# Performance work log

Hardware: AMD Instinct MI355X
Metric: run time of the kernel (lower is better)

## Reference

```python
import jax, jax.numpy as jnp
import numpy as np

N, F_IN, HID, H1, E = 50000, 512, 128, 4, 800000
NEG_SLOPE = 0.2

def setup_inputs() -> dict:
    key = jax.random.key(0)
    ks = jax.random.split(key, 10)
    s = lambda fan: 1.0 / np.sqrt(fan)
    x = jax.random.normal(ks[0], (N, F_IN), jnp.float32)
    edge_index = jax.random.randint(ks[1], (2, E), 0, N, jnp.int32)
    W1 = jax.random.normal(ks[2], (F_IN, H1 * HID), jnp.float32) * s(F_IN)
    a_src1 = jax.random.normal(ks[3], (H1, HID), jnp.float32) * s(HID)
    a_dst1 = jax.random.normal(ks[4], (H1, HID), jnp.float32) * s(HID)
    b1 = jnp.zeros((H1 * HID,), jnp.float32)
    W2 = jax.random.normal(ks[5], (H1 * HID, HID), jnp.float32) * s(H1 * HID)
    a_src2 = jax.random.normal(ks[6], (1, HID), jnp.float32) * s(HID)
    a_dst2 = jax.random.normal(ks[7], (1, HID), jnp.float32) * s(HID)
    b2 = jnp.zeros((HID,), jnp.float32)
    return {"x": x, "edge_index": edge_index, "W1": W1, "a_src1": a_src1,
            "a_dst1": a_dst1, "b1": b1, "W2": W2, "a_src2": a_src2,
            "a_dst2": a_dst2, "b2": b2}

def _gat(x, src, dst, W, a_src, a_dst, b, n):
    H, C = a_src.shape
    h = (x @ W).reshape(-1, H, C)                      # [N, H, C]
    # per-edge attention logits: alpha_src[src] + alpha_dst[dst]
    e = jax.nn.leaky_relu((h * a_src).sum(-1)[src] + (h * a_dst).sum(-1)[dst],
                          NEG_SLOPE)                   # [E', H]
    # segment softmax over destination node
    m = jax.ops.segment_max(e, dst, num_segments=n)
    p = jnp.exp(e - m[dst])
    denom = jax.ops.segment_sum(p, dst, num_segments=n)
    alpha = p / (denom[dst] + 1e-16)
    # weighted scatter-add aggregation
    out = jax.ops.segment_sum(h[src] * alpha[:, :, None], dst, num_segments=n)
    return out.reshape(-1, H * C) + b

def reference(x, edge_index, W1, a_src1, a_dst1, b1, W2, a_src2, a_dst2, b2):
    loops = jnp.arange(N, dtype=edge_index.dtype)      # add_self_loops=True
    src = jnp.concatenate([edge_index[0], loops])
    dst = jnp.concatenate([edge_index[1], loops])
    h = jax.nn.elu(_gat(x, src, dst, W1, a_src1, a_dst1, b1, N))
    return _gat(h, src, dst, W2, a_src2, a_dst2, b2, N)
```

## Files before the change

kernel.cpp:

```cpp
#include <hip/hip_runtime.h>
#include <hip/hip_bf16.h>
#include <math.h>

#define NEG_SLOPE 0.2f

constexpr int N_NODES = 50000;
constexpr int F_IN    = 512;
constexpr int HID     = 128;
constexpr int H1      = 4;
constexpr int E_EDGES = 800000;
constexpr int E_TOT   = E_EDGES + N_NODES;
constexpr int DEG_CAP = 64;

typedef __attribute__((ext_vector_type(8))) short short8;
typedef __attribute__((ext_vector_type(4))) float floatx4;
typedef __attribute__((ext_vector_type(2))) float f32x2;
typedef __attribute__((ext_vector_type(4))) unsigned short ushort4v;
typedef __attribute__((ext_vector_type(8))) unsigned short ushort8v;

__device__ __forceinline__ unsigned short f2bf(float f) {
  union { float f; unsigned int u; } v; v.f = f;
  unsigned int u = v.u + 0x7FFFu + ((v.u >> 16) & 1u);
  return (unsigned short)(u >> 16);
}
__device__ __forceinline__ float bf_lo(unsigned int u) {
  union { unsigned int u; float f; } v; v.u = u << 16; return v.f;
}
__device__ __forceinline__ float bf_hi(unsigned int u) {
  union { unsigned int u; float f; } v; v.u = u & 0xFFFF0000u; return v.f;
}

template <int CPT>
__device__ __forceinline__ void store_vec(unsigned short* p, const float* v) {
#pragma unroll
  for (int c = 0; c < CPT; c += 4) {
    ushort4v o;
#pragma unroll
    for (int j = 0; j < 4; ++j) o[j] = f2bf(v[c + j]);
    *(ushort4v*)(p + c) = o;
  }
}
template <int CPT>
__device__ __forceinline__ void store_vec(float* p, const float* v) {
#pragma unroll
  for (int c = 0; c < CPT; c += 4) *(float4*)(p + c) = *(const float4*)(v + c);
}

__device__ __forceinline__ void async_load16(const void* g, void* lds) {
  __builtin_amdgcn_global_load_lds(
      (const __attribute__((address_space(1))) unsigned int*)g,
      (__attribute__((address_space(3))) unsigned int*)lds, 16, 0, 0);
}

__global__ void prep_kernel(const float* __restrict__ W1, const float* __restrict__ W2,
                            unsigned short* __restrict__ W1t, unsigned short* __restrict__ W2t,
                            int* __restrict__ cnt) {
  int i = blockIdx.x * 256 + threadIdx.x;
  if (i < N_NODES) cnt[i] = 0;
  int j = i - N_NODES;
  if (j >= 0 && j < 512 * 512) {
    int n = j >> 9, k = j & 511;
    W1t[j] = f2bf(W1[k * 512 + n]);
  }
  int l = i - N_NODES - 512 * 512;
  if (l >= 0 && l < 128 * 512) {
    int n = l >> 9, k = l & 511;
    W2t[l] = f2bf(W2[k * 128 + n]);
  }
}

template <bool CVT_A, bool FILL>
__global__ __launch_bounds__(256) void gemm_bf16_kernel(
    const void* __restrict__ Araw, const unsigned short* __restrict__ Bt,
    unsigned short* __restrict__ C, const float* __restrict__ a_srcp,
    const float* __restrict__ a_dstp,
    float* __restrict__ alpha_src, float* __restrict__ alpha_dst,
    int M, int N, int K, int Hn, int nRowTiles,
    const int* __restrict__ ei, int* __restrict__ cnt, int* __restrict__ adj,
    int gemmBlocks) {
  __shared__ unsigned short As[128 * 32];
  __shared__ unsigned short Bs[128 * 32];
  __shared__ unsigned short Cs[128 * 132];
  __shared__ float red_s[128][2];
  __shared__ float red_d[128][2];

  if (FILL && blockIdx.x >= gemmBlocks) {
    int i = (blockIdx.x - gemmBlocks) * 256 + threadIdx.x;
    if (i < E_TOT) {
      int s, d;
      if (i < E_EDGES) { s = ei[i]; d = ei[E_EDGES + i]; }
      else             { s = i - E_EDGES; d = s; }
      int pos = atomicAdd(&cnt[d], 1);
      if (pos < DEG_CAP) adj[d * DEG_CAP + pos] = s;
    }
    return;
  }

  int grp = blockIdx.x / (8 * Hn);
  int w8 = blockIdx.x % (8 * Hn);
  int head = w8 >> 3;
  int rowTile = grp * 8 + (w8 & 7);
  if (rowTile >= nRowTiles) return;
  int row0 = rowTile * 128;
  int col0 = head * 128;

  int tid = threadIdx.x;
  int lane = tid & 63, wave = tid >> 6;
  int wm = wave & 1, wn = wave >> 1;
  int l15 = lane & 15, quad = lane >> 4;

  floatx4 acc[4][4];
#pragma unroll
  for (int i = 0; i < 4; ++i)
#pragma unroll
    for (int j = 0; j < 4; ++j) acc[i][j] = (floatx4){0.f, 0.f, 0.f, 0.f};

  int seg_b = wave * 2;
  int r_in = (lane >> 2);
  int c8sw = (((lane & 3) ^ ((lane >> 3) & 3)) * 8);
  int sqrd = (quad ^ ((l15 >> 1) & 3)) * 8;

  for (int k0 = 0; k0 < K; k0 += 32) {
#pragma unroll
    for (int p = 0; p < 2; ++p) {
      int seg = seg_b + p;
      int r = seg * 16 + r_in;
      int gc = col0 + r;
      async_load16(Bt + (size_t)gc * K + k0 + c8sw, &Bs[seg * 512]);
    }
    if constexpr (CVT_A) {
      const float* Af = (const float*)Araw;
#pragma unroll
      for (int p = 0; p < 4; ++p) {
        int lin = tid + p * 256;
        int r = lin >> 3;
        int q = lin & 7;
        int gr = row0 + r; if (gr >= M) gr = M - 1;
        float4 f = *(const float4*)(Af + (size_t)gr * K + k0 + q * 4);
        ushort4v o;
        o[0] = f2bf(f.x); o[1] = f2bf(f.y); o[2] = f2bf(f.z); o[3] = f2bf(f.w);
        int sl = ((q >> 1) ^ ((lin >> 4) & 3));
        *(ushort4v*)&As[r * 32 + sl * 8 + (q & 1) * 4] = o;
      }
    } else {
      const unsigned short* Ab = (const unsigned short*)Araw;
#pragma unroll
      for (int p = 0; p < 2; ++p) {
        int seg = seg_b + p;
        int r = seg * 16 + r_in;
        int gr = row0 + r; if (gr >= M) gr = M - 1;
        async_load16(Ab + (size_t)gr * K + k0 + c8sw, &As[seg * 512]);
      }
    }
    __syncthreads();

    short8 a[4], b[4];
#pragma unroll
    for (int mi = 0; mi < 4; ++mi)
      a[mi] = *(const short8*)&As[(wm * 64 + mi * 16 + l15) * 32 + sqrd];
#pragma unroll
    for (int ni = 0; ni < 4; ++ni)
      b[ni] = *(const short8*)&Bs[(wn * 64 + ni * 16 + l15) * 32 + sqrd];
#pragma unroll
    for (int mi = 0; mi < 4; ++mi)
#pragma unroll
      for (int ni = 0; ni < 4; ++ni)
        acc[mi][ni] = __builtin_amdgcn_mfma_f32_16x16x32_bf16(a[mi], b[ni], acc[mi][ni], 0, 0, 0);
    __syncthreads();
  }

  float a_s[4], a_d[4];
#pragma unroll
  for (int ni = 0; ni < 4; ++ni) {
    int cih = wn * 64 + ni * 16 + l15;
    a_s[ni] = a_srcp[head * HID + cih];
    a_d[ni] = a_dstp[head * HID + cih];
  }

#pragma unroll
  for (int mi = 0; mi < 4; ++mi) {
#pragma unroll
    for (int r = 0; r < 4; ++r) {
      int rloc = wm * 64 + mi * 16 + quad * 4 + r;
      float ps = 0.f, pd = 0.f;
#pragma unroll
      for (int ni = 0; ni < 4; ++ni) {
        float v = acc[mi][ni][r];
        ps += v * a_s[ni];
        pd += v * a_d[ni];
        Cs[rloc * 132 + wn * 64 + ni * 16 + l15] = f2bf(v);
      }
#pragma unroll
      for (int off = 1; off < 16; off <<= 1) {
        ps += __shfl_xor(ps, off);
        pd += __shfl_xor(pd, off);
      }
      if (l15 == 0) { red_s[rloc][wn] = ps; red_d[rloc][wn] = pd; }
    }
  }
  __syncthreads();

  {
    int row = tid >> 1;
    int cc  = (tid & 1) * 64;
    int grow = row0 + row;
    if (grow < M) {
      const unsigned short* src = &Cs[row * 132 + cc];
      unsigned short* dst = &C[(size_t)grow * N + col0 + cc];
#pragma unroll
      for (int c = 0; c < 64; c += 8)
        *(ushort8v*)(dst + c) = *(const ushort8v*)(src + c);
    }
  }
  if (tid < 128) {
    int grow = row0 + tid;
    if (grow < M) {
      alpha_src[(size_t)grow * Hn + head] = red_s[tid][0] + red_s[tid][1];
      alpha_dst[(size_t)grow * Hn + head] = red_d[tid][0] + red_d[tid][1];
    }
  }
}

template <int H, typename OT>
__global__ __launch_bounds__(64) void aggregate_kernel(
    const unsigned short* __restrict__ h, const float* __restrict__ asrc,
    const float* __restrict__ adst, const int* __restrict__ cnt,
    const int* __restrict__ adj, const float* __restrict__ bias,
    OT* __restrict__ out, int apply_elu) {
  constexpr int CPT = 8;
  constexpr int CH = H * HID;
  constexpr int NCH = CH / CPT;
  constexpr int SLOTS = 64 / NCH;
  __shared__ float p_sh[64 * H];
  __shared__ int ro_sh[64];

  const int node = blockIdx.x;
  const int lane = threadIdx.x;
  int deg = cnt[node];
  if (deg > DEG_CAP) deg = DEG_CAP;

  int s_i = 0;
  if (lane < deg) s_i = adj[node * DEG_CAP + lane];
  ro_sh[lane] = s_i * (CH * 2);
  float ar[H];
  if constexpr (H == 4) {
    float4 f = (lane < deg) ? *(const float4*)(asrc + (size_t)s_i * 4)
                            : make_float4(0.f, 0.f, 0.f, 0.f);
    ar[0] = f.x; ar[1] = f.y; ar[2] = f.z; ar[3] = f.w;
  } else {
    ar[0] = (lane < deg) ? asrc[s_i] : 0.f;
  }
  asm volatile("s_waitcnt lgkmcnt(0)" ::: "memory");

  const int chlane = lane % NCH;
  const int slot = lane / NCH;
  const int ch = chlane * CPT;
  const int head = ch >> 7;
  const char* hb = (const char*)h + ch * 2;

  auto loadu = [&](uint4& U, int e) {
    if (e < deg) U = *(const uint4*)(hb + (unsigned)ro_sh[e]);
    else         U = make_uint4(0u, 0u, 0u, 0u);
  };

  uint4 u0, u1, u2, u3, u4, u5, u6, u7;
  loadu(u0, slot);             loadu(u1, slot + SLOTS);
  loadu(u2, slot + 2 * SLOTS); loadu(u3, slot + 3 * SLOTS);
  loadu(u4, slot + 4 * SLOTS); loadu(u5, slot + 5 * SLOTS);
  loadu(u6, slot + 6 * SLOTS); loadu(u7, slot + 7 * SLOTS);

#pragma unroll
  for (int hh = 0; hh < H; ++hh) {
    float v = ar[hh] + adst[node * H + hh];
    v = (v > 0.f) ? v : NEG_SLOPE * v;
    float lg = (lane < deg) ? v : -1e30f;
#pragma unroll
    for (int o = 32; o; o >>= 1) lg = fmaxf(lg, __shfl_xor(lg, o));
    float p = (lane < deg) ? __expf(v - lg) : 0.f;
    float s = p;
#pragma unroll
    for (int o = 32; o; o >>= 1) s += __shfl_xor(s, o);
    p_sh[lane * H + hh] = p * (1.f / (s + 1e-16f));
  }
  asm volatile("s_waitcnt lgkmcnt(0)" ::: "memory");

  f32x2 ac0 = {0.f, 0.f}, ac1 = {0.f, 0.f}, ac2v = {0.f, 0.f}, ac3 = {0.f, 0.f};
  auto consume = [&](const uint4& U, int e) {
    float w = p_sh[(e & 63) * H + head];
    f32x2 wp = {w, w};
    f32x2 t;
    t.x = bf_lo(U.x); t.y = bf_hi(U.x); ac0  += t * wp;
    t.x = bf_lo(U.y); t.y = bf_hi(U.y); ac1  += t * wp;
    t.x = bf_lo(U.z); t.y = bf_hi(U.z); ac2v += t * wp;
    t.x = bf_lo(U.w); t.y = bf_hi(U.w); ac3  += t * wp;
  };

  int base = 0;
  for (;;) {
    int nb = base + 8 * SLOTS;
    if (nb < deg) {
      consume(u0, base + slot);             loadu(u0, nb + slot);
      consume(u1, base + slot + SLOTS);     loadu(u1, nb + slot + SLOTS);
      consume(u2, base + slot + 2 * SLOTS); loadu(u2, nb + slot + 2 * SLOTS);
      consume(u3, base + slot + 3 * SLOTS); loadu(u3, nb + slot + 3 * SLOTS);
      consume(u4, base + slot + 4 * SLOTS); loadu(u4, nb + slot + 4 * SLOTS);
      consume(u5, base + slot + 5 * SLOTS); loadu(u5, nb + slot + 5 * SLOTS);
      consume(u6, base + slot + 6 * SLOTS); loadu(u6, nb + slot + 6 * SLOTS);
      consume(u7, base + slot + 7 * SLOTS); loadu(u7, nb + slot + 7 * SLOTS);
      base = nb;
    } else {
      consume(u0, base + slot);             consume(u1, base + slot + SLOTS);
      consume(u2, base + slot + 2 * SLOTS); consume(u3, base + slot + 3 * SLOTS);
      consume(u4, base + slot + 4 * SLOTS); consume(u5, base + slot + 5 * SLOTS);
      consume(u6, base + slot + 6 * SLOTS); consume(u7, base + slot + 7 * SLOTS);
      break;
    }
  }

#pragma unroll
  for (int o = NCH; o < 64; o <<= 1) {
    ac0.x  += __shfl_xor(ac0.x, o);  ac0.y  += __shfl_xor(ac0.y, o);
    ac1.x  += __shfl_xor(ac1.x, o);  ac1.y  += __shfl_xor(ac1.y, o);
    ac2v.x += __shfl_xor(ac2v.x, o); ac2v.y += __shfl_xor(ac2v.y, o);
    ac3.x  += __shfl_xor(ac3.x, o);  ac3.y  += __shfl_xor(ac3.y, o);
  }

  if (slot == 0) {
    float r[CPT] = {ac0.x, ac0.y, ac1.x, ac1.y, ac2v.x, ac2v.y, ac3.x, ac3.y};
#pragma unroll
    for (int c = 0; c < CPT; ++c) {
      float t = r[c] + bias[ch + c];
      if (apply_elu) t = (t > 0.f) ? t : (__expf(t) - 1.f);
      r[c] = t;
    }
    store_vec<CPT>(&out[(size_t)node * CH + ch], r);
  }
}

extern "C" void kernel_launch(void* const* d_in, const int* in_sizes, int n_in,
                              void* d_out, int out_size, void* d_ws, size_t ws_size,
                              hipStream_t stream) {
  const float* x      = (const float*)d_in[0];
  const int*   ei     = (const int*)d_in[1];
  const float* W1     = (const float*)d_in[2];
  const float* a_src1 = (const float*)d_in[3];
  const float* a_dst1 = (const float*)d_in[4];
  const float* b1     = (const float*)d_in[5];
  const float* W2     = (const float*)d_in[6];
  const float* a_src2 = (const float*)d_in[7];
  const float* a_dst2 = (const float*)d_in[8];
  const float* b2     = (const float*)d_in[9];
  float* out = (float*)d_out;

  float* ws   = (float*)d_ws;
  float* as1  = ws;
  float* ad1  = as1 + N_NODES * H1;
  float* as2  = ad1 + N_NODES * H1;
  float* ad2  = as2 + N_NODES;
  unsigned short* bufA = (unsigned short*)(ad2 + N_NODES);
  unsigned short* bufB = bufA + (size_t)N_NODES * 512;
  unsigned short* hmidb = bufA;
  unsigned short* h1b   = bufB;
  unsigned short* h2b   = bufB;
  unsigned short* W1t   = bufB + (size_t)N_NODES * 512;
  unsigned short* W2t   = W1t + 512 * 512;
  int* cnt = (int*)(W2t + 128 * 512);
  int* adj = cnt + N_NODES;

  constexpr int NRT = (N_NODES + 127) / 128;
  constexpr int NRT8 = ((NRT + 7) / 8) * 8;
  constexpr int PREP_ITEMS = N_NODES + 512 * 512 + 128 * 512;
  constexpr int FILL_BLOCKS = (E_TOT + 255) / 256;
  constexpr int GEMM1_BLOCKS = NRT8 * H1;

  prep_kernel<<<(PREP_ITEMS + 255) / 256, 256, 0, stream>>>(W1, W2, W1t, W2t, cnt);

  gemm_bf16_kernel<true, true>
      <<<GEMM1_BLOCKS + FILL_BLOCKS, 256, 0, stream>>>(
      x, W1t, h1b, a_src1, a_dst1, as1, ad1, N_NODES, 512, 512, H1, NRT,
      ei, cnt, adj, GEMM1_BLOCKS);
  aggregate_kernel<4, unsigned short><<<N_NODES, 64, 0, stream>>>(
      h1b, as1, ad1, cnt, adj, b1, hmidb, 1);

  gemm_bf16_kernel<false, false><<<NRT8, 256, 0, stream>>>(
      hmidb, W2t, h2b, a_src2, a_dst2, as2, ad2, N_NODES, 128, 512, 1, NRT,
      nullptr, nullptr, nullptr, 0);
  aggregate_kernel<1, float><<<N_NODES, 64, 0, stream>>>(
      h2b, as2, ad2, cnt, adj, b2, out, 0);
}
```

Before: 464.0 us.

## Pre-convert x to bf16 in prep kernel and alias GEMM LDS buffers

```diff
diff --git a/kernel.cpp b/kernel.cpp
--- a/kernel.cpp
+++ b/kernel.cpp
@@ -52,35 +52,51 @@
       (__attribute__((address_space(3))) unsigned int*)lds, 16, 0, 0);
 }
 
-__global__ void prep_kernel(const float* __restrict__ W1, const float* __restrict__ W2,
+constexpr int XC8 = N_NODES * F_IN / 8;
+__global__ void prep_kernel(const float* __restrict__ x, unsigned short* __restrict__ xb,
+                            const float* __restrict__ W1, const float* __restrict__ W2,
                             unsigned short* __restrict__ W1t, unsigned short* __restrict__ W2t,
                             int* __restrict__ cnt) {
   int i = blockIdx.x * 256 + threadIdx.x;
-  if (i < N_NODES) cnt[i] = 0;
-  int j = i - N_NODES;
-  if (j >= 0 && j < 512 * 512) {
+  if (i < XC8) {
+    int i8 = i * 8;
+    float4 f0 = *(const float4*)(x + i8);
+    float4 f1 = *(const float4*)(x + i8 + 4);
+    ushort8v o;
+    o[0] = f2bf(f0.x); o[1] = f2bf(f0.y); o[2] = f2bf(f0.z); o[3] = f2bf(f0.w);
+    o[4] = f2bf(f1.x); o[5] = f2bf(f1.y); o[6] = f2bf(f1.z); o[7] = f2bf(f1.w);
+    *(ushort8v*)(xb + i8) = o;
+    return;
+  }
+  int j = i - XC8;
+  if (j < 512 * 512) {
     int n = j >> 9, k = j & 511;
     W1t[j] = f2bf(W1[k * 512 + n]);
-  }
-  int l = i - N_NODES - 512 * 512;
-  if (l >= 0 && l < 128 * 512) {
+    return;
+  }
+  int l = j - 512 * 512;
+  if (l < 128 * 512) {
     int n = l >> 9, k = l & 511;
     W2t[l] = f2bf(W2[k * 128 + n]);
-  }
-}
-
-template <bool CVT_A, bool FILL>
+    return;
+  }
+  int c = l - 128 * 512;
+  if (c < N_NODES) cnt[c] = 0;
+}
+
+template <bool FILL>
 __global__ __launch_bounds__(256) void gemm_bf16_kernel(
-    const void* __restrict__ Araw, const unsigned short* __restrict__ Bt,
+    const unsigned short* __restrict__ A, const unsigned short* __restrict__ Bt,
     unsigned short* __restrict__ C, const float* __restrict__ a_srcp,
     const float* __restrict__ a_dstp,
     float* __restrict__ alpha_src, float* __restrict__ alpha_dst,
     int M, int N, int K, int Hn, int nRowTiles,
     const int* __restrict__ ei, int* __restrict__ cnt, int* __restrict__ adj,
     int gemmBlocks) {
-  __shared__ unsigned short As[128 * 32];
-  __shared__ unsigned short Bs[128 * 32];
-  __shared__ unsigned short Cs[128 * 132];
+  __shared__ __align__(16) unsigned char smem[128 * 132 * 2];
+  unsigned short* As = (unsigned short*)smem;
+  unsigned short* Bs = (unsigned short*)(smem + 8192);
+  unsigned short* Cs = (unsigned short*)smem;
   __shared__ float red_s[128][2];
   __shared__ float red_d[128][2];
 
@@ -128,29 +144,12 @@
       int gc = col0 + r;
       async_load16(Bt + (size_t)gc * K + k0 + c8sw, &Bs[seg * 512]);
     }
-    if constexpr (CVT_A) {
-      const float* Af = (const float*)Araw;
-#pragma unroll
-      for (int p = 0; p < 4; ++p) {
-        int lin = tid + p * 256;
-        int r = lin >> 3;
-        int q = lin & 7;
-        int gr = row0 + r; if (gr >= M) gr = M - 1;
-        float4 f = *(const float4*)(Af + (size_t)gr * K + k0 + q * 4);
-        ushort4v o;
-        o[0] = f2bf(f.x); o[1] = f2bf(f.y); o[2] = f2bf(f.z); o[3] = f2bf(f.w);
-        int sl = ((q >> 1) ^ ((lin >> 4) & 3));
-        *(ushort4v*)&As[r * 32 + sl * 8 + (q & 1) * 4] = o;
-      }
-    } else {
-      const unsigned short* Ab = (const unsigned short*)Araw;
-#pragma unroll
-      for (int p = 0; p < 2; ++p) {
-        int seg = seg_b + p;
-        int r = seg * 16 + r_in;
-        int gr = row0 + r; if (gr >= M) gr = M - 1;
-        async_load16(Ab + (size_t)gr * K + k0 + c8sw, &As[seg * 512]);
-      }
+#pragma unroll
+    for (int p = 0; p < 2; ++p) {
+      int seg = seg_b + p;
+      int r = seg * 16 + r_in;
+      int gr = row0 + r; if (gr >= M) gr = M - 1;
+      async_load16(A + (size_t)gr * K + k0 + c8sw, &As[seg * 512]);
     }
     __syncthreads();
 
@@ -359,6 +358,7 @@
   float* ad2  = as2 + N_NODES;
   unsigned short* bufA = (unsigned short*)(ad2 + N_NODES);
   unsigned short* bufB = bufA + (size_t)N_NODES * 512;
+  unsigned short* xbf   = bufA;
   unsigned short* hmidb = bufA;
   unsigned short* h1b   = bufB;
   unsigned short* h2b   = bufB;
@@ -369,20 +369,20 @@
 
   constexpr int NRT = (N_NODES + 127) / 128;
   constexpr int NRT8 = ((NRT + 7) / 8) * 8;
-  constexpr int PREP_ITEMS = N_NODES + 512 * 512 + 128 * 512;
+  constexpr int PREP_ITEMS = XC8 + 512 * 512 + 128 * 512 + N_NODES;
   constexpr int FILL_BLOCKS = (E_TOT + 255) / 256;
   constexpr int GEMM1_BLOCKS = NRT8 * H1;
 
-  prep_kernel<<<(PREP_ITEMS + 255) / 256, 256, 0, stream>>>(W1, W2, W1t, W2t, cnt);
-
-  gemm_bf16_kernel<true, true>
-      <<<GEMM1_BLOCKS + FILL_BLOCKS, 256, 0, stream>>>(
-      x, W1t, h1b, a_src1, a_dst1, as1, ad1, N_NODES, 512, 512, H1, NRT,
+  prep_kernel<<<(PREP_ITEMS + 255) / 256, 256, 0, stream>>>(
+      x, xbf, W1, W2, W1t, W2t, cnt);
+
+  gemm_bf16_kernel<true><<<GEMM1_BLOCKS + FILL_BLOCKS, 256, 0, stream>>>(
+      xbf, W1t, h1b, a_src1, a_dst1, as1, ad1, N_NODES, 512, 512, H1, NRT,
       ei, cnt, adj, GEMM1_BLOCKS);
   aggregate_kernel<4, unsigned short><<<N_NODES, 64, 0, stream>>>(
       h1b, as1, ad1, cnt, adj, b1, hmidb, 1);
 
-  gemm_bf16_kernel<false, false><<<NRT8, 256, 0, stream>>>(
+  gemm_bf16_kernel<false><<<NRT8, 256, 0, stream>>>(
       hmidb, W2t, h2b, a_src2, a_dst2, as2, ad2, N_NODES, 128, 512, 1, NRT,
       nullptr, nullptr, nullptr, 0);
   aggregate_kernel<1, float><<<N_NODES, 64, 0, stream>>>(
```

Result: slower. 487.0 us (+5.0%).

## Double-buffer GEMM LDS tiles and prefetch the next K-step during MFMA

Applied to the files above, without the earlier changes.

```diff
diff --git a/kernel.cpp b/kernel.cpp
--- a/kernel.cpp
+++ b/kernel.cpp
@@ -78,9 +78,12 @@
     int M, int N, int K, int Hn, int nRowTiles,
     const int* __restrict__ ei, int* __restrict__ cnt, int* __restrict__ adj,
     int gemmBlocks) {
-  __shared__ unsigned short As[128 * 32];
-  __shared__ unsigned short Bs[128 * 32];
-  __shared__ unsigned short Cs[128 * 132];
+  __shared__ __align__(16) unsigned char smem[128 * 132 * 2];
+  unsigned short* As0 = (unsigned short*)smem;
+  unsigned short* As1 = (unsigned short*)(smem + 8192);
+  unsigned short* Bs0 = (unsigned short*)(smem + 16384);
+  unsigned short* Bs1 = (unsigned short*)(smem + 24576);
+  unsigned short* Cs  = (unsigned short*)smem;
   __shared__ float red_s[128][2];
   __shared__ float red_d[128][2];
 
@@ -120,7 +123,10 @@
   int c8sw = (((lane & 3) ^ ((lane >> 3) & 3)) * 8);
   int sqrd = (quad ^ ((l15 >> 1) & 3)) * 8;
 
-  for (int k0 = 0; k0 < K; k0 += 32) {
+  const float* Af = (const float*)Araw;
+  const unsigned short* Ab = (const unsigned short*)Araw;
+
+  auto stageB = [&](int k0, unsigned short* Bs) {
 #pragma unroll
     for (int p = 0; p < 2; ++p) {
       int seg = seg_b + p;
@@ -128,45 +134,92 @@
       int gc = col0 + r;
       async_load16(Bt + (size_t)gc * K + k0 + c8sw, &Bs[seg * 512]);
     }
-    if constexpr (CVT_A) {
-      const float* Af = (const float*)Araw;
-#pragma unroll
-      for (int p = 0; p < 4; ++p) {
-        int lin = tid + p * 256;
-        int r = lin >> 3;
-        int q = lin & 7;
-        int gr = row0 + r; if (gr >= M) gr = M - 1;
-        float4 f = *(const float4*)(Af + (size_t)gr * K + k0 + q * 4);
-        ushort4v o;
-        o[0] = f2bf(f.x); o[1] = f2bf(f.y); o[2] = f2bf(f.z); o[3] = f2bf(f.w);
-        int sl = ((q >> 1) ^ ((lin >> 4) & 3));
-        *(ushort4v*)&As[r * 32 + sl * 8 + (q & 1) * 4] = o;
+  };
+  auto stageA_async = [&](int k0, unsigned short* As) {
+#pragma unroll
+    for (int p = 0; p < 2; ++p) {
+      int seg = seg_b + p;
+      int r = seg * 16 + r_in;
+      int gr = row0 + r; if (gr >= M) gr = M - 1;
+      async_load16(Ab + (size_t)gr * K + k0 + c8sw, &As[seg * 512]);
+    }
+  };
+
+  float4 fA[4];
+  auto loadA_regs = [&](int k0) {
+#pragma unroll
+    for (int p = 0; p < 4; ++p) {
+      int lin = tid + p * 256;
+      int r = lin >> 3;
+      int q = lin & 7;
+      int gr = row0 + r; if (gr >= M) gr = M - 1;
+      fA[p] = *(const float4*)(Af + (size_t)gr * K + k0 + q * 4);
+    }
+  };
+  auto writeA_lds = [&](unsigned short* As) {
+#pragma unroll
+    for (int p = 0; p < 4; ++p) {
+      int lin = tid + p * 256;
+      int r = lin >> 3;
+      int q = lin & 7;
+      ushort4v o;
+      o[0] = f2bf(fA[p].x); o[1] = f2bf(fA[p].y); o[2] = f2bf(fA[p].z); o[3] = f2bf(fA[p].w);
+      int sl = ((q >> 1) ^ ((lin >> 4) & 3));
+      *(ushort4v*)&As[r * 32 + sl * 8 + (q & 1) * 4] = o;
+    }
+  };
+
+  const int nsteps = K >> 5;
+
+  stageB(0, Bs0);
+  if constexpr (CVT_A) {
+    loadA_regs(0);
+    writeA_lds(As0);
+    if (nsteps > 1) loadA_regs(32);
+    asm volatile("s_waitcnt lgkmcnt(0)" ::: "memory");
+  } else {
+    stageA_async(0, As0);
+    asm volatile("s_waitcnt vmcnt(0)" ::: "memory");
+  }
+  __builtin_amdgcn_s_barrier();
+
+  for (int t = 0; t < nsteps; ++t) {
+    int cur = t & 1;
+    unsigned short* Asc = cur ? As1 : As0;
+    unsigned short* Bsc = cur ? Bs1 : Bs0;
+    unsigned short* Asn = cur ? As0 : As1;
+    unsigned short* Bsn = cur ? Bs0 : Bs1;
+    int k1 = (t + 1) << 5;
+
+    if (t + 1 < nsteps) {
+      stageB(k1, Bsn);
+      if constexpr (CVT_A) {
+        writeA_lds(Asn);
+        if (t + 2 < nsteps) loadA_regs(k1 + 32);
+        asm volatile("s_waitcnt lgkmcnt(4)" ::: "memory");
+      } else {
+        stageA_async(k1, Asn);
+        asm volatile("s_waitcnt vmcnt(4)" ::: "memory");
       }
     } else {
-      const unsigned short* Ab = (const unsigned short*)Araw;
-#pragma unroll
-      for (int p = 0; p < 2; ++p) {
-        int seg = seg_b + p;
-        int r = seg * 16 + r_in;
-        int gr = row0 + r; if (gr >= M) gr = M - 1;
-        async_load16(Ab + (size_t)gr * K + k0 + c8sw, &As[seg * 512]);
-      }
-    }
-    __syncthreads();
+      asm volatile("s_waitcnt vmcnt(0) lgkmcnt(0)" ::: "memory");
+    }
+    __builtin_amdgcn_s_barrier();
 
     short8 a[4], b[4];
 #pragma unroll
     for (int mi = 0; mi < 4; ++mi)
-      a[mi] = *(const short8*)&As[(wm * 64 + mi * 16 + l15) * 32 + sqrd];
+      a[mi] = *(const short8*)&Asc[(wm * 64 + mi * 16 + l15) * 32 + sqrd];
 #pragma unroll
     for (int ni = 0; ni < 4; ++ni)
-      b[ni] = *(const short8*)&Bs[(wn * 64 + ni * 16 + l15) * 32 + sqrd];
+      b[ni] = *(const short8*)&Bsc[(wn * 64 + ni * 16 + l15) * 32 + sqrd];
 #pragma unroll
     for (int mi = 0; mi < 4; ++mi)
 #pragma unroll
       for (int ni = 0; ni < 4; ++ni)
         acc[mi][ni] = __builtin_amdgcn_mfma_f32_16x16x32_bf16(a[mi], b[ni], acc[mi][ni], 0, 0, 0);
-    __syncthreads();
+
+    __builtin_amdgcn_s_barrier();
   }
 
   float a_s[4], a_d[4];
```

Result: slower. 495.4 us (+6.8%).
